# Kernel tuning notes

Measured on AMD Instinct MI355X. Metric: run time of the kernel, lower is better.

## Reference

```python
import jax, jax.numpy as jnp
import numpy as np

D_MODEL = 256
NUM_HEADS = 8
CURV = 1.0  # Poincare ball curvature c
EPS = 1e-5


def expmap0(v, c):
    # Exponential map at the origin of the Poincare ball.
    sqrt_c = jnp.sqrt(c)
    norm = jnp.sqrt(jnp.clip(jnp.sum(v * v, axis=-1, keepdims=True), 1e-12))
    return jnp.tanh(sqrt_c * norm) * v / (sqrt_c * norm)


def setup_inputs() -> dict:
    key = jax.random.key(0)
    ks = jax.random.split(key, 12)
    B, S, D = 2, 2048, D_MODEL
    s = 1.0 / np.sqrt(D)
    return {
        "x": jax.random.normal(ks[0], (B, S, D), dtype=jnp.float32),
        "Wq": jax.random.normal(ks[1], (D, D), dtype=jnp.float32) * s,
        "bq": jnp.zeros((D,), jnp.float32),
        "Wk": jax.random.normal(ks[2], (D, D), dtype=jnp.float32) * s,
        "bk": jnp.zeros((D,), jnp.float32),
        "Wv": jax.random.normal(ks[3], (D, D), dtype=jnp.float32) * s,
        "bv": jnp.zeros((D,), jnp.float32),
        "Wo": jax.random.normal(ks[4], (D, D), dtype=jnp.float32) * s,
        "bo": jnp.zeros((D,), jnp.float32),
        "Wfc": jax.random.normal(ks[5], (D, D), dtype=jnp.float32) * s,
        "bfc": jnp.zeros((D,), jnp.float32),
    }


def reference(x, Wq, bq, Wk, bk, Wv, bv, Wo, bo, Wfc, bfc):
    B, S, D = x.shape
    H, dh = NUM_HEADS, D // NUM_HEADS
    c = CURV

    def proj(W, b):
        return (x @ W.T + b).reshape(B, S, H, dh).transpose(0, 2, 1, 3)  # [B,H,S,dh]

    q = expmap0(proj(Wq, bq), c)
    k = expmap0(proj(Wk, bk), c)
    v = proj(Wv, bv)

    # Gram quantities; pairwise Poincare distance via closed-form Mobius-add norm.
    qq = jnp.sum(q * q, axis=-1)[..., :, None]          # [B,H,S,1]
    kk = jnp.sum(k * k, axis=-1)[..., None, :]          # [B,H,1,S]
    qk = jnp.einsum("bhsd,bhtd->bhst", q, k)            # [B,H,S,S]

    A = 1.0 - 2.0 * c * qk + c * kk
    Bc = 1.0 - c * qq
    den = 1.0 - 2.0 * c * qk + (c * c) * qq * kk
    num2 = A * A * qq + Bc * Bc * kk - 2.0 * A * Bc * qk  # ||(-q) mobius+ k||^2 * den^2
    n = jnp.sqrt(jnp.clip(num2, 0.0)) / jnp.clip(jnp.abs(den), 1e-12)
    sqrt_c = jnp.sqrt(c)
    dist = (2.0 / sqrt_c) * jnp.arctanh(jnp.clip(sqrt_c * n, 0.0, 1.0 - EPS))

    scores = -dist / np.sqrt(dh)
    attn = jax.nn.softmax(scores, axis=-1)
    out = jnp.einsum("bhst,bhtd->bhsd", attn, v)        # [B,H,S,dh]
    out = out.transpose(0, 2, 1, 3).reshape(B, S, D)
    out = out @ Wo.T + bo
    return out @ Wfc.T + bfc
```

## Files before the change

kernel.cpp:

```cpp
#include <hip/hip_runtime.h>
#include <cstdint>
#include <cstddef>


#define ALPHA 0.17677669529663687f
#define EMIN  -3.1129694f
#define CHI   1.95e-5f
#define NEG_INV_2CHI -25641.026f

typedef __bf16 bf16x8 __attribute__((ext_vector_type(8)));
typedef float  f32x4  __attribute__((ext_vector_type(4)));

__device__ __forceinline__ float fast_log2(float x) { return __builtin_amdgcn_logf(x); }
__device__ __forceinline__ float fast_exp2(float x) { return __builtin_amdgcn_exp2f(x); }

__global__ __launch_bounds__(256)
void k1_misc(const float* __restrict__ x,   const float* __restrict__ Wq,
             const float* __restrict__ Wk,  const float* __restrict__ Wv,
             const float* __restrict__ Wfc, const float* __restrict__ Wo,
             const float* __restrict__ bo,  const float* __restrict__ bfc,
             __bf16* __restrict__ xh, __bf16* __restrict__ xl,
             __bf16* __restrict__ Ws, __bf16* __restrict__ Wch,
             __bf16* __restrict__ Wcl, float* __restrict__ bcomb) {
  __shared__ float sh[2 * 32 * 68];
  const int bx = blockIdx.x, tid = threadIdx.x;
  if (bx < 16) {
    float (*AsT)[68] = (float(*)[68])sh;
    float (*Bs)[68]  = (float(*)[68])(sh + 32 * 68);
    const int ty = tid >> 4, tx = tid & 15;
    const int m0 = (bx >> 2) * 64, n0 = (bx & 3) * 64;
    float acc[4][4] = {};
    for (int k0 = 0; k0 < 256; k0 += 32) {
#pragma unroll
      for (int jj = 0; jj < 2; ++jj) {
        int j = tid * 2 + jj;
        {
          int r = j >> 3, c4 = (j & 7) << 2;
          float4 av = *(const float4*)&Wfc[(size_t)(m0 + r) * 256 + k0 + c4];
          AsT[c4 + 0][r] = av.x; AsT[c4 + 1][r] = av.y;
          AsT[c4 + 2][r] = av.z; AsT[c4 + 3][r] = av.w;
        }
        {
          int r = j >> 4, c4 = (j & 15) << 2;
          *(float4*)&Bs[r][c4] = *(const float4*)&Wo[(size_t)(k0 + r) * 256 + n0 + c4];
        }
      }
      __syncthreads();
#pragma unroll
      for (int kk = 0; kk < 32; ++kk) {
        float4 a = *(const float4*)&AsT[kk][ty * 4];
        float4 b = *(const float4*)&Bs[kk][tx * 4];
        float av[4] = {a.x, a.y, a.z, a.w};
        float bv[4] = {b.x, b.y, b.z, b.w};
#pragma unroll
        for (int i = 0; i < 4; ++i)
#pragma unroll
          for (int j2 = 0; j2 < 4; ++j2)
            acc[i][j2] = fmaf(av[i], bv[j2], acc[i][j2]);
      }
      __syncthreads();
    }
#pragma unroll
    for (int i = 0; i < 4; ++i) {
      union { __bf16 h[4]; uint2 u; } ph, pl;
#pragma unroll
      for (int j = 0; j < 4; ++j) {
        __bf16 hb = (__bf16)acc[i][j];
        ph.h[j] = hb;
        pl.h[j] = (__bf16)(acc[i][j] - (float)hb);
      }
      size_t off = (size_t)(m0 + ty * 4 + i) * 256 + n0 + tx * 4;
      *(uint2*)(Wch + off) = ph.u;
      *(uint2*)(Wcl + off) = pl.u;
    }
  } else if (bx < 32) {
    float* red = sh;
    int r = tid >> 4, c = tid & 15;
    int row = (bx - 16) * 16 + r;
    float s = 0.0f;
    for (int k = c; k < 256; k += 16) s = fmaf(Wfc[(size_t)row * 256 + k], bo[k], s);
    red[tid] = s;
    __syncthreads();
    if (c == 0) {
      float t = 0.0f;
#pragma unroll
      for (int i = 0; i < 16; ++i) t += red[r * 16 + i];
      bcomb[row] = t + bfc[row];
    }
  } else {
    int g = (bx - 32) * 256 + tid;
    const float* src;
    __bf16 *dh, *dl;
    if (g < 131072) {
      src = x + (size_t)g * 8; dh = xh + (size_t)g * 8; dl = xl + (size_t)g * 8;
    } else {
      int e = g - 131072;
      int wsel = e >> 13;
      int inner = (e & 8191) * 8;
      src = (wsel == 0 ? Wq : (wsel == 1 ? Wk : Wv)) + inner;
      dh = Ws + wsel * 131072 + inner;
      dl = Ws + wsel * 131072 + 65536 + inner;
    }
    union { __bf16 h[8]; uint4 u; } ph, pl;
#pragma unroll
    for (int i = 0; i < 2; ++i) {
      float4 v = *(const float4*)(src + i * 4);
      float vv[4] = {v.x, v.y, v.z, v.w};
#pragma unroll
      for (int j = 0; j < 4; ++j) {
        __bf16 hb = (__bf16)vv[j];
        ph.h[i * 4 + j] = hb;
        pl.h[i * 4 + j] = (__bf16)(vv[j] - (float)hb);
      }
    }
    *(uint4*)dh = ph.u;
    *(uint4*)dl = pl.u;
  }
}

__global__ __launch_bounds__(256)
void gemm_qkv_mfma(const __bf16* __restrict__ xh, const __bf16* __restrict__ xl,
                   const __bf16* __restrict__ Ws,
                   const float* __restrict__ bq, const float* __restrict__ bk,
                   const float* __restrict__ bv,
                   float* __restrict__ Qb, float* __restrict__ Kb,
                   float* __restrict__ Vb) {
  const int tid = threadIdx.x, w = tid >> 6, lane = tid & 63;
  const int l15 = lane & 15, lg = lane >> 4;
  const int m0 = blockIdx.x * 64, nb = blockIdx.y;
  const int wsel = nb >> 2;
  const int n256b = (nb & 3) * 64;
  const __bf16* Wh = Ws + wsel * 131072;
  const __bf16* Wl = Wh + 65536;
  const int arow = m0 + w * 16 + l15;
  const __bf16* axh = xh + (size_t)arow * 256 + lg * 8;
  const __bf16* axl = xl + (size_t)arow * 256 + lg * 8;
  f32x4 acc0 = {0,0,0,0}, acc1 = {0,0,0,0}, acc2 = {0,0,0,0}, acc3 = {0,0,0,0};
#pragma unroll
  for (int k0 = 0; k0 < 256; k0 += 32) {
    bf16x8 ah = *(const bf16x8*)(axh + k0);
    bf16x8 al = *(const bf16x8*)(axl + k0);
#pragma unroll
    for (int g = 0; g < 4; ++g) {
      const size_t br = (size_t)(n256b + g * 16 + l15) * 256 + lg * 8 + k0;
      bf16x8 bh = *(const bf16x8*)(Wh + br);
      bf16x8 bl = *(const bf16x8*)(Wl + br);
      f32x4& acc = g == 0 ? acc0 : (g == 1 ? acc1 : (g == 2 ? acc2 : acc3));
      acc = __builtin_amdgcn_mfma_f32_16x16x32_bf16(ah, bh, acc, 0, 0, 0);
      acc = __builtin_amdgcn_mfma_f32_16x16x32_bf16(al, bh, acc, 0, 0, 0);
      acc = __builtin_amdgcn_mfma_f32_16x16x32_bf16(ah, bl, acc, 0, 0, 0);
    }
  }
  const float* bias = wsel == 0 ? bq : (wsel == 1 ? bk : bv);
  float* C = wsel == 0 ? Qb : (wsel == 1 ? Kb : Vb);
#pragma unroll
  for (int g = 0; g < 4; ++g) {
    const f32x4& acc = g == 0 ? acc0 : (g == 1 ? acc1 : (g == 2 ? acc2 : acc3));
    int n256 = n256b + g * 16 + l15;
    float bval = bias[n256];
    int h = n256 >> 5, d = n256 & 31;
#pragma unroll
    for (int r = 0; r < 4; ++r) {
      int m = m0 + w * 16 + lg * 4 + r;
      int b = m >> 11, s = m & 2047;
      C[((size_t)((b << 3) + h) << 16) + (size_t)s * 32 + d] = acc[r] + bval;
    }
  }
}

__global__ __launch_bounds__(256)
void k3_prep(const float* __restrict__ Qf, const float* __restrict__ Kf,
             const float* __restrict__ Vf,
             __bf16* __restrict__ Qbf, __bf16* __restrict__ Kbf,
             __bf16* __restrict__ Vt,
             float4* __restrict__ qtab4, float4* __restrict__ ktab4,
             float* __restrict__ Vsum, float2* __restrict__ Kred) {
  __shared__ float2 red2[256];
  const int bx = blockIdx.x, tid = threadIdx.x;
  if (bx < 256) {
    int idx = bx * 256 + tid;
    const bool isQ = idx < 32768;
    const int i2 = isQ ? idx : idx - 32768;
    const float* src = (isQ ? Qf : Kf) + (size_t)i2 * 32;
    __bf16* dst = (isQ ? Qbf : Kbf) + (size_t)i2 * 32;
    float v[32];
    float ss = 0.0f;
#pragma unroll
    for (int i = 0; i < 8; ++i) {
      float4 v4 = *(const float4*)&src[i * 4];
      v[i*4+0] = v4.x; v[i*4+1] = v4.y; v[i*4+2] = v4.z; v[i*4+3] = v4.w;
      ss = fmaf(v4.x, v4.x, ss); ss = fmaf(v4.y, v4.y, ss);
      ss = fmaf(v4.z, v4.z, ss); ss = fmaf(v4.w, v4.w, ss);
    }
    ss = fmaxf(ss, 1e-12f);
    float x  = sqrtf(ss);
    float ex = fast_exp2(-2.8853900817779268f * x);
    float opex = 1.0f + ex;
    float th = (1.0f - ex) / opex;
    float sc = th / x;
    float qq = th * th;
    float Bv = 4.0f * ex / (opex * opex);
    float lgB = 2.0f - 2.8853900817779268f * x - 2.0f * fast_log2(opex);
    if (isQ) qtab4[i2] = float4{qq, ALPHA * lgB, Bv, 0.0f};
    else     ktab4[i2] = float4{qq, Bv, ALPHA * lgB, 0.0f};
    union { __bf16 h[8]; uint4 u; } pk;
#pragma unroll
    for (int blk = 0; blk < 4; ++blk) {
#pragma unroll
      for (int j = 0; j < 8; ++j) pk.h[j] = (__bf16)(v[blk * 8 + j] * sc);
      *(uint4*)(dst + blk * 8) = pk.u;
    }
    if (!isQ) {
      red2[tid] = float2{qq, Bv};
      __syncthreads();
      for (int s = 128; s > 0; s >>= 1) {
        if (tid < s) {
          red2[tid].x = fminf(red2[tid].x, red2[tid + s].x);
          red2[tid].y = fmaxf(red2[tid].y, red2[tid + s].y);
        }
        __syncthreads();
      }
      if (tid == 0) Kred[bx - 128] = red2[0];
    }
  } else if (bx < 768) {
    int g = (bx - 256) * 256 + tid;
    int bh = g >> 13, rem = g & 8191;
    int tb = rem >> 5, dh = rem & 31;
    const float* src = Vf + (((size_t)bh * 2048 + tb * 8) * 32) + dh;
    union { __bf16 h[8]; uint4 u; } pk;
#pragma unroll
    for (int e = 0; e < 8; ++e) pk.h[e] = (__bf16)src[e * 32];
    *(uint4*)(Vt + ((size_t)bh * 32 + dh) * 2048 + tb * 8) = pk.u;
  } else {
    int g = (bx - 768) * 256 + tid;
    int bh = g >> 11, rem = g & 2047;
    int t32 = rem >> 5, dh = rem & 31;
    const float* src = Vf + (((size_t)bh * 2048 + t32 * 32) * 32) + dh;
    float s = 0.0f;
#pragma unroll
    for (int j = 0; j < 32; ++j) s += src[j * 32];
    Vsum[((size_t)bh * 64 + t32) * 32 + dh] = s;
  }
}

__global__ __launch_bounds__(256)
void attn_mfma(const __bf16* __restrict__ Qbf, const __bf16* __restrict__ Kbf,
               const __bf16* __restrict__ Vt,  const float4* __restrict__ qtab4,
               const float4* __restrict__ ktab4, const float* __restrict__ Vsum,
               const float2* __restrict__ Kred,
               float* __restrict__ PN, float* __restrict__ PD) {
  __shared__ __bf16 Pt[4][16][72];
  const int tid = threadIdx.x;
  const int wid = tid >> 6, lane = tid & 63;
  const int l15 = lane & 15, lg = lane >> 4;
  const int tc = blockIdx.y, bh = blockIdx.z;
  const int sblk = blockIdx.x;
  const int s0 = sblk * 64 + wid * 16;

  bf16x8 qfrag = *(const bf16x8*)(Qbf + ((size_t)bh * 2048 + s0 + l15) * 32 + lg * 8);
  float4 qt = qtab4[bh * 2048 + s0 + l15];
  const float qq = qt.x, Bq = qt.z;
  const float eminRow = EMIN - qt.y;
  const float wclipf = (float)(__bf16)fast_exp2(eminRow);
  float wrow[4];
#pragma unroll
  for (int r = 0; r < 4; ++r)
    wrow[r] = (float)(__bf16)fast_exp2(EMIN - qtab4[bh * 2048 + s0 + lg * 4 + r].y);

  float kkmin = 1.0f, bkmax = 0.0f;
#pragma unroll
  for (int j = 0; j < 8; ++j) {
    float2 kr = Kred[bh * 8 + j];
    kkmin = fminf(kkmin, kr.x);
    bkmax = fmaxf(bkmax, kr.y);
  }
  const float thr_all = fmaf(0.5f * qq, kkmin,
                             fmaf(Bq * NEG_INV_2CHI, bkmax, 0.5f));

  const __bf16* Kbase = Kbf + ((size_t)bh << 16);
  const __bf16* Vbase = Vt + ((size_t)bh << 16);
  const float4* Tk = ktab4 + bh * 2048;
  const float*  VsBase = Vsum + (size_t)bh * 64 * 32;
  __bf16* Pw = &Pt[wid][0][0];

  f32x4 accO0 = {0.f, 0.f, 0.f, 0.f};
  f32x4 accO1 = {0.f, 0.f, 0.f, 0.f};
  float den = 0.0f;
  int nclip = 0;
  const f32x4 zero = {0.f, 0.f, 0.f, 0.f};
  const int tbeg = tc * 512;
  const int stag = sblk & 7;

  bf16x8 kfA0, kfA1, kfA2, kfA3, kfB0, kfB1, kfB2, kfB3;
  float vA0, vA1, vA2, vA3, vB0, vB1, vB2, vB3;

#define LOAD_SET(K0, K1, K2, K3, V0, V1, V2, V3, T0)                          \
  {                                                                           \
    const int _t = (T0);                                                      \
    K0 = *(const bf16x8*)(Kbase + (size_t)(_t + 0 * 16 + l15) * 32 + lg * 8); \
    K1 = *(const bf16x8*)(Kbase + (size_t)(_t + 1 * 16 + l15) * 32 + lg * 8); \
    K2 = *(const bf16x8*)(Kbase + (size_t)(_t + 2 * 16 + l15) * 32 + lg * 8); \
    K3 = *(const bf16x8*)(Kbase + (size_t)(_t + 3 * 16 + l15) * 32 + lg * 8); \
    const int _ti = _t >> 5;                                                  \
    V0 = VsBase[_ti * 32 + l15];                                              \
    V1 = VsBase[(_ti + 1) * 32 + l15];                                        \
    V2 = VsBase[_ti * 32 + 16 + l15];                                         \
    V3 = VsBase[(_ti + 1) * 32 + 16 + l15];                                   \
  }

#define COMPUTE_SET(K0, K1, K2, K3, V0, V1, V2, V3, T0)                       \
  {                                                                           \
    const int _t0 = (T0);                                                     \
    __builtin_amdgcn_s_setprio(1);                                            \
    _Pragma("unroll")                                                         \
    for (int h = 0; h < 2; ++h) {                                             \
      f32x4 S[2];                                                             \
      bool ok = true;                                                         \
      _Pragma("unroll")                                                       \
      for (int s2 = 0; s2 < 2; ++s2) {                                        \
        bf16x8 kf = (h == 0) ? (s2 == 0 ? K0 : K1) : (s2 == 0 ? K2 : K3);     \
        f32x4 Sv = __builtin_amdgcn_mfma_f32_16x16x32_bf16(kf, qfrag, zero,   \
                                                           0, 0, 0);          \
        S[s2] = Sv;                                                           \
        float m = fmaxf(fmaxf(Sv[0], Sv[1]), fmaxf(Sv[2], Sv[3]));            \
        ok &= (m <= thr_all);                                                 \
      }                                                                       \
      if (__all((int)ok)) {                                                   \
        ++nclip;                                                              \
        const float vsA = h ? V1 : V0;                                        \
        const float vsB = h ? V3 : V2;                                        \
        _Pragma("unroll")                                                     \
        for (int r = 0; r < 4; ++r) {                                         \
          accO0[r] = fmaf(wrow[r], vsA, accO0[r]);                            \
          accO1[r] = fmaf(wrow[r], vsB, accO1[r]);                            \
        }                                                                     \
      } else {                                                                \
        _Pragma("unroll")                                                     \
        for (int s2 = 0; s2 < 2; ++s2) {                                      \
          const int sub = h * 2 + s2;                                         \
          const int tk = _t0 + sub * 16 + lg * 4;                             \
          f32x4 Sv = S[s2];                                                   \
          float w[4];                                                         \
          _Pragma("unroll")                                                   \
          for (int r = 0; r < 4; ++r) {                                       \
            float4 T = Tk[tk + r];                                            \
            float qk2 = Sv[r] + Sv[r];                                        \
            float u = (qq + T.x) - qk2;                                       \
            float d = fmaf(qq, T.x, 1.0f) - qk2;                              \
            float p = fmaxf(u * d, 0.0f);                                     \
            float sq = sqrtf(p);                                              \
            float m2 = fmaf(2.0f, sq, u + d);                                 \
            float e = fmaf(-ALPHA, fast_log2(m2), T.z);                       \
            e = fmaxf(e, eminRow);                                            \
            w[r] = fast_exp2(e);                                              \
          }                                                                   \
          den += (w[0] + w[1]) + (w[2] + w[3]);                               \
          union { __bf16 hh[4]; uint2 u2; } pk;                               \
          pk.hh[0] = (__bf16)w[0]; pk.hh[1] = (__bf16)w[1];                   \
          pk.hh[2] = (__bf16)w[2]; pk.hh[3] = (__bf16)w[3];                   \
          *(uint2*)&Pw[l15 * 72 + sub * 16 + lg * 4] = pk.u2;                 \
        }                                                                     \
        bf16x8 pfrag = *(const bf16x8*)&Pw[l15 * 72 + h * 32 + lg * 8];       \
        bf16x8 v0 = *(const bf16x8*)(Vbase + (size_t)l15 * 2048 + _t0 +       \
                                     h * 32 + lg * 8);                        \
        bf16x8 v1 = *(const bf16x8*)(Vbase + (size_t)(16 + l15) * 2048 +      \
                                     _t0 + h * 32 + lg * 8);                  \
        accO0 = __builtin_amdgcn_mfma_f32_16x16x32_bf16(pfrag, v0, accO0,     \
                                                        0, 0, 0);             \
        accO1 = __builtin_amdgcn_mfma_f32_16x16x32_bf16(pfrag, v1, accO1,     \
                                                        0, 0, 0);             \
      }                                                                       \
    }                                                                         \
    __builtin_amdgcn_s_setprio(0);                                            \
  }

  LOAD_SET(kfA0, kfA1, kfA2, kfA3, vA0, vA1, vA2, vA3,
           tbeg + ((stag & 7) << 6));

#pragma unroll
  for (int i = 0; i < 8; ++i) {
    const int tcur = tbeg + (((i + stag) & 7) << 6);
    const int tnxt = tbeg + (((i + 1 + stag) & 7) << 6);
    if ((i & 1) == 0) {
      if (i < 7) LOAD_SET(kfB0, kfB1, kfB2, kfB3, vB0, vB1, vB2, vB3, tnxt);
      COMPUTE_SET(kfA0, kfA1, kfA2, kfA3, vA0, vA1, vA2, vA3, tcur);
    } else {
      if (i < 7) LOAD_SET(kfA0, kfA1, kfA2, kfA3, vA0, vA1, vA2, vA3, tnxt);
      COMPUTE_SET(kfB0, kfB1, kfB2, kfB3, vB0, vB1, vB2, vB3, tcur);
    }
  }
#undef LOAD_SET
#undef COMPUTE_SET

  den = fmaf(8.0f * wclipf, (float)nclip, den);
  den += __shfl_xor(den, 16);
  den += __shfl_xor(den, 32);
  size_t pbase = ((size_t)tc * 16 + bh) * 2048;
  if (lg == 0) PD[pbase + s0 + l15] = den;
#pragma unroll
  for (int r = 0; r < 4; ++r) {
    int sl = lg * 4 + r;
    size_t row = (pbase + s0 + sl) * 32;
    PN[row + l15]      = accO0[r];
    PN[row + 16 + l15] = accO1[r];
  }
}

__global__ __launch_bounds__(256)
void combine4(const float* __restrict__ PN, const float* __restrict__ PD,
              __bf16* __restrict__ AOh, __bf16* __restrict__ AOl) {
  int idx = blockIdx.x * 256 + threadIdx.x;
  int bh = idx >> 11, s = idx & 2047;
  int b = bh >> 3, h = bh & 7;
  float den = 0.0f;
#pragma unroll
  for (int c = 0; c < 4; ++c) den += PD[((size_t)c * 16 + bh) * 2048 + s];
  float r = 1.0f / den;
  size_t ob = ((size_t)b * 2048 + s) * 256 + h * 32;
#pragma unroll
  for (int i = 0; i < 8; ++i) {
    float4 sum = {0.0f, 0.0f, 0.0f, 0.0f};
#pragma unroll
    for (int c = 0; c < 4; ++c) {
      float4 v = *(const float4*)&PN[((((size_t)c * 16 + bh) * 2048 + s) * 32) + i * 4];
      sum.x += v.x; sum.y += v.y; sum.z += v.z; sum.w += v.w;
    }
    float vv[4] = {sum.x * r, sum.y * r, sum.z * r, sum.w * r};
    union { __bf16 h4[4]; uint2 u; } ph, pl;
#pragma unroll
    for (int j = 0; j < 4; ++j) {
      __bf16 hb = (__bf16)vv[j];
      ph.h4[j] = hb;
      pl.h4[j] = (__bf16)(vv[j] - (float)hb);
    }
    *(uint2*)(AOh + ob + i * 4) = ph.u;
    *(uint2*)(AOl + ob + i * 4) = pl.u;
  }
}

__global__ __launch_bounds__(256)
void gemm_out_mfma(const __bf16* __restrict__ aoh, const __bf16* __restrict__ aol,
                   const __bf16* __restrict__ Wch, const __bf16* __restrict__ Wcl,
                   const float* __restrict__ bcomb, float* __restrict__ out) {
  const int tid = threadIdx.x, w = tid >> 6, lane = tid & 63;
  const int l15 = lane & 15, lg = lane >> 4;
  const int m0 = blockIdx.x * 64, n0 = blockIdx.y * 64;
  const int arow = m0 + w * 16 + l15;
  const __bf16* axh = aoh + (size_t)arow * 256 + lg * 8;
  const __bf16* axl = aol + (size_t)arow * 256 + lg * 8;
  f32x4 acc0 = {0,0,0,0}, acc1 = {0,0,0,0}, acc2 = {0,0,0,0}, acc3 = {0,0,0,0};
#pragma unroll
  for (int k0 = 0; k0 < 256; k0 += 32) {
    bf16x8 ah = *(const bf16x8*)(axh + k0);
    bf16x8 al = *(const bf16x8*)(axl + k0);
#pragma unroll
    for (int g = 0; g < 4; ++g) {
      const size_t br = (size_t)(n0 + g * 16 + l15) * 256 + lg * 8 + k0;
      bf16x8 bh = *(const bf16x8*)(Wch + br);
      bf16x8 bl = *(const bf16x8*)(Wcl + br);
      f32x4& acc = g == 0 ? acc0 : (g == 1 ? acc1 : (g == 2 ? acc2 : acc3));
      acc = __builtin_amdgcn_mfma_f32_16x16x32_bf16(ah, bh, acc, 0, 0, 0);
      acc = __builtin_amdgcn_mfma_f32_16x16x32_bf16(al, bh, acc, 0, 0, 0);
      acc = __builtin_amdgcn_mfma_f32_16x16x32_bf16(ah, bl, acc, 0, 0, 0);
    }
  }
#pragma unroll
  for (int g = 0; g < 4; ++g) {
    const f32x4& acc = g == 0 ? acc0 : (g == 1 ? acc1 : (g == 2 ? acc2 : acc3));
    int n = n0 + g * 16 + l15;
    float bval = bcomb[n];
#pragma unroll
    for (int r = 0; r < 4; ++r) {
      int m = m0 + w * 16 + lg * 4 + r;
      out[(size_t)m * 256 + n] = acc[r] + bval;
    }
  }
}

extern "C" void kernel_launch(void* const* d_in, const int* in_sizes, int n_in,
                              void* d_out, int out_size, void* d_ws, size_t ws_size,
                              hipStream_t stream) {
  const float* x   = (const float*)d_in[0];
  const float* Wq  = (const float*)d_in[1];
  const float* bq  = (const float*)d_in[2];
  const float* Wk  = (const float*)d_in[3];
  const float* bk  = (const float*)d_in[4];
  const float* Wv  = (const float*)d_in[5];
  const float* bv  = (const float*)d_in[6];
  const float* Wo  = (const float*)d_in[7];
  const float* bo  = (const float*)d_in[8];
  const float* Wfc = (const float*)d_in[9];
  const float* bfc = (const float*)d_in[10];

  float* ws = (float*)d_ws;
  float* Qb  = ws;
  float* Kb  = ws + (1 << 20);
  float* Vb  = ws + (2 << 20);
  __bf16* Qbf = (__bf16*)(ws + (3 << 20));
  __bf16* Kbf = (__bf16*)(ws + (3 << 20) + (1 << 19));
  __bf16* Vtb = (__bf16*)(ws + (4 << 20));
  float4* qtab4 = (float4*)(ws + (4 << 20) + (1 << 19));
  float4* ktab4 = (float4*)(ws + (4 << 20) + (1 << 19) + (1 << 17));
  float*  Vsum  = ws + (4 << 20) + (1 << 19) + (2 << 17);
  __bf16* Wch   = (__bf16*)(Vsum + (1 << 15));
  __bf16* Wcl   = Wch + 65536;
  float*  bcomb = Vsum + (1 << 15) + (1 << 16);
  float2* Kred  = (float2*)(bcomb + 256);
  __bf16* xh = (__bf16*)(ws + (5 << 20));
  __bf16* xl = (__bf16*)(ws + (5 << 20) + (1 << 19));
  __bf16* Wsplit = (__bf16*)(ws + (6 << 20));
  float* PN = ws + (6 << 20) + (1 << 18);
  float* PD = PN + (4 << 20);
  __bf16* AOh = (__bf16*)ws;
  __bf16* AOl = (__bf16*)(ws + (1 << 19));

  dim3 blk(256);
  k1_misc<<<dim3(640), blk, 0, stream>>>(x, Wq, Wk, Wv, Wfc, Wo, bo, bfc,
                                         xh, xl, Wsplit, Wch, Wcl, bcomb);
  gemm_qkv_mfma<<<dim3(64, 12), blk, 0, stream>>>(xh, xl, Wsplit, bq, bk, bv,
                                                  Qb, Kb, Vb);
  k3_prep<<<dim3(896), blk, 0, stream>>>(Qb, Kb, Vb, Qbf, Kbf, Vtb,
                                         qtab4, ktab4, Vsum, Kred);
  attn_mfma<<<dim3(32, 4, 16), blk, 0, stream>>>(Qbf, Kbf, Vtb, qtab4, ktab4,
                                                 Vsum, Kred, PN, PD);
  combine4<<<dim3(128), blk, 0, stream>>>(PN, PD, AOh, AOl);
  gemm_out_mfma<<<dim3(64, 4), blk, 0, stream>>>(AOh, AOl, Wch, Wcl, bcomb,
                                                 (float*)d_out);
}
```

Baseline: 110.1 us.

## Fuse expmap0 Q/K prep into QKV GEMM epilogue and store partials in bf16

The QKV GEMM epilogue now applies the bias and computes per-head norms with cross-lane shuffles. It then applies the expmap0 scaling and writes bf16 Q/K, the q/k tables and the K min/max reduction directly, so fp32 Q/K no longer round-trip through global memory. The V transpose and sum move to a smaller dedicated kernel. Attention partial numerators are stored as bf16 instead of fp32, halving combine traffic but adding rounding error in the partial sums.

Result: faster. 105.8 us (-3.9%).

```diff
diff --git a/kernel.cpp b/kernel.cpp
--- a/kernel.cpp
+++ b/kernel.cpp
@@ -7,6 +7,7 @@
 #define EMIN  -3.1129694f
 #define CHI   1.95e-5f
 #define NEG_INV_2CHI -25641.026f
+#define TWOLOG2E 2.8853900817779268f
 
 typedef __bf16 bf16x8 __attribute__((ext_vector_type(8)));
 typedef float  f32x4  __attribute__((ext_vector_type(4)));
@@ -123,8 +124,11 @@
                    const __bf16* __restrict__ Ws,
                    const float* __restrict__ bq, const float* __restrict__ bk,
                    const float* __restrict__ bv,
-                   float* __restrict__ Qb, float* __restrict__ Kb,
-                   float* __restrict__ Vb) {
+                   __bf16* __restrict__ Qbf, __bf16* __restrict__ Kbf,
+                   float* __restrict__ Vb,
+                   float4* __restrict__ qtab4, float4* __restrict__ ktab4,
+                   float2* __restrict__ Kred) {
+  __shared__ float4 kredsh[4];
   const int tid = threadIdx.x, w = tid >> 6, lane = tid & 63;
   const int l15 = lane & 15, lg = lane >> 4;
   const int m0 = blockIdx.x * 64, nb = blockIdx.y;
@@ -152,78 +156,125 @@
     }
   }
   const float* bias = wsel == 0 ? bq : (wsel == 1 ? bk : bv);
-  float* C = wsel == 0 ? Qb : (wsel == 1 ? Kb : Vb);
-#pragma unroll
-  for (int g = 0; g < 4; ++g) {
-    const f32x4& acc = g == 0 ? acc0 : (g == 1 ? acc1 : (g == 2 ? acc2 : acc3));
-    int n256 = n256b + g * 16 + l15;
-    float bval = bias[n256];
-    int h = n256 >> 5, d = n256 & 31;
+
+  if (wsel == 2) {
+#pragma unroll
+    for (int g = 0; g < 4; ++g) {
+      const f32x4& acc = g == 0 ? acc0 : (g == 1 ? acc1 : (g == 2 ? acc2 : acc3));
+      int n256 = n256b + g * 16 + l15;
+      float bval = bias[n256];
+      int h = n256 >> 5, d = n256 & 31;
+#pragma unroll
+      for (int r = 0; r < 4; ++r) {
+        int m = m0 + w * 16 + lg * 4 + r;
+        int b = m >> 11, s = m & 2047;
+        Vb[((size_t)((b << 3) + h) << 16) + (size_t)s * 32 + d] = acc[r] + bval;
+      }
+    }
+    return;
+  }
+
+  const float bv0 = bias[n256b + 0 * 16 + l15];
+  const float bv1 = bias[n256b + 1 * 16 + l15];
+  const float bv2 = bias[n256b + 2 * 16 + l15];
+  const float bv3 = bias[n256b + 3 * 16 + l15];
+  float ssA[4], ssB[4];
+#pragma unroll
+  for (int r = 0; r < 4; ++r) {
+    acc0[r] += bv0; acc1[r] += bv1; acc2[r] += bv2; acc3[r] += bv3;
+    ssA[r] = acc0[r] * acc0[r] + acc1[r] * acc1[r];
+    ssB[r] = acc2[r] * acc2[r] + acc3[r] * acc3[r];
+  }
+#pragma unroll
+  for (int mk = 1; mk < 16; mk <<= 1) {
 #pragma unroll
     for (int r = 0; r < 4; ++r) {
-      int m = m0 + w * 16 + lg * 4 + r;
-      int b = m >> 11, s = m & 2047;
-      C[((size_t)((b << 3) + h) << 16) + (size_t)s * 32 + d] = acc[r] + bval;
+      ssA[r] += __shfl_xor(ssA[r], mk);
+      ssB[r] += __shfl_xor(ssB[r], mk);
+    }
+  }
+  float scA[4], qqA[4], BvA[4], lgA[4];
+  float scB[4], qqB[4], BvB[4], lgB_[4];
+#pragma unroll
+  for (int r = 0; r < 4; ++r) {
+    {
+      float ss = fmaxf(ssA[r], 1e-12f);
+      float xv = sqrtf(ss);
+      float ex = fast_exp2(-TWOLOG2E * xv);
+      float opex = 1.0f + ex;
+      float th = (1.0f - ex) / opex;
+      scA[r] = th / xv;
+      qqA[r] = th * th;
+      BvA[r] = 4.0f * ex / (opex * opex);
+      lgA[r] = 2.0f - TWOLOG2E * xv - 2.0f * fast_log2(opex);
+    }
+    {
+      float ss = fmaxf(ssB[r], 1e-12f);
+      float xv = sqrtf(ss);
+      float ex = fast_exp2(-TWOLOG2E * xv);
+      float opex = 1.0f + ex;
+      float th = (1.0f - ex) / opex;
+      scB[r] = th / xv;
+      qqB[r] = th * th;
+      BvB[r] = 4.0f * ex / (opex * opex);
+      lgB_[r] = 2.0f - TWOLOG2E * xv - 2.0f * fast_log2(opex);
+    }
+  }
+  __bf16* dst = wsel == 0 ? Qbf : Kbf;
+  float4* tab = wsel == 0 ? qtab4 : ktab4;
+  const int b = m0 >> 11;
+  const int headA = n256b >> 5, headB = headA + 1;
+  const int bhA = (b << 3) + headA, bhB = (b << 3) + headB;
+  const int sbase = (m0 & 2047) + w * 16 + lg * 4;
+#pragma unroll
+  for (int r = 0; r < 4; ++r) {
+    int s = sbase + r;
+    size_t baseA = ((size_t)bhA * 2048 + s) * 32;
+    size_t baseB = ((size_t)bhB * 2048 + s) * 32;
+    dst[baseA + l15]      = (__bf16)(acc0[r] * scA[r]);
+    dst[baseA + 16 + l15] = (__bf16)(acc1[r] * scA[r]);
+    dst[baseB + l15]      = (__bf16)(acc2[r] * scB[r]);
+    dst[baseB + 16 + l15] = (__bf16)(acc3[r] * scB[r]);
+    if (l15 == 0) {
+      if (wsel == 0) {
+        tab[(size_t)bhA * 2048 + s] = float4{qqA[r], ALPHA * lgA[r], BvA[r], 0.0f};
+        tab[(size_t)bhB * 2048 + s] = float4{qqB[r], ALPHA * lgB_[r], BvB[r], 0.0f};
+      } else {
+        tab[(size_t)bhA * 2048 + s] = float4{qqA[r], BvA[r], ALPHA * lgA[r], 0.0f};
+        tab[(size_t)bhB * 2048 + s] = float4{qqB[r], BvB[r], ALPHA * lgB_[r], 0.0f};
+      }
+    }
+  }
+  if (wsel == 1) {
+    float mnA = fminf(fminf(qqA[0], qqA[1]), fminf(qqA[2], qqA[3]));
+    float mxA = fmaxf(fmaxf(BvA[0], BvA[1]), fmaxf(BvA[2], BvA[3]));
+    float mnB = fminf(fminf(qqB[0], qqB[1]), fminf(qqB[2], qqB[3]));
+    float mxB = fmaxf(fmaxf(BvB[0], BvB[1]), fmaxf(BvB[2], BvB[3]));
+    mnA = fminf(mnA, __shfl_xor(mnA, 16)); mnA = fminf(mnA, __shfl_xor(mnA, 32));
+    mxA = fmaxf(mxA, __shfl_xor(mxA, 16)); mxA = fmaxf(mxA, __shfl_xor(mxA, 32));
+    mnB = fminf(mnB, __shfl_xor(mnB, 16)); mnB = fminf(mnB, __shfl_xor(mnB, 32));
+    mxB = fmaxf(mxB, __shfl_xor(mxB, 16)); mxB = fmaxf(mxB, __shfl_xor(mxB, 32));
+    if (lane == 0) kredsh[w] = float4{mnA, mxA, mnB, mxB};
+    __syncthreads();
+    if (tid == 0) {
+      float4 a = kredsh[0], b4 = kredsh[1], c4 = kredsh[2], d4 = kredsh[3];
+      float MnA = fminf(fminf(a.x, b4.x), fminf(c4.x, d4.x));
+      float MxA = fmaxf(fmaxf(a.y, b4.y), fmaxf(c4.y, d4.y));
+      float MnB = fminf(fminf(a.z, b4.z), fminf(c4.z, d4.z));
+      float MxB = fmaxf(fmaxf(a.w, b4.w), fmaxf(c4.w, d4.w));
+      int bx31 = blockIdx.x & 31;
+      Kred[bhA * 32 + bx31] = float2{MnA, MxA};
+      Kred[bhB * 32 + bx31] = float2{MnB, MxB};
     }
   }
 }
 
 __global__ __launch_bounds__(256)
-void k3_prep(const float* __restrict__ Qf, const float* __restrict__ Kf,
-             const float* __restrict__ Vf,
-             __bf16* __restrict__ Qbf, __bf16* __restrict__ Kbf,
-             __bf16* __restrict__ Vt,
-             float4* __restrict__ qtab4, float4* __restrict__ ktab4,
-             float* __restrict__ Vsum, float2* __restrict__ Kred) {
-  __shared__ float2 red2[256];
+void k3v(const float* __restrict__ Vf, __bf16* __restrict__ Vt,
+         float* __restrict__ Vsum) {
   const int bx = blockIdx.x, tid = threadIdx.x;
-  if (bx < 256) {
-    int idx = bx * 256 + tid;
-    const bool isQ = idx < 32768;
-    const int i2 = isQ ? idx : idx - 32768;
-    const float* src = (isQ ? Qf : Kf) + (size_t)i2 * 32;
-    __bf16* dst = (isQ ? Qbf : Kbf) + (size_t)i2 * 32;
-    float v[32];
-    float ss = 0.0f;
-#pragma unroll
-    for (int i = 0; i < 8; ++i) {
-      float4 v4 = *(const float4*)&src[i * 4];
-      v[i*4+0] = v4.x; v[i*4+1] = v4.y; v[i*4+2] = v4.z; v[i*4+3] = v4.w;
-      ss = fmaf(v4.x, v4.x, ss); ss = fmaf(v4.y, v4.y, ss);
-      ss = fmaf(v4.z, v4.z, ss); ss = fmaf(v4.w, v4.w, ss);
-    }
-    ss = fmaxf(ss, 1e-12f);
-    float x  = sqrtf(ss);
-    float ex = fast_exp2(-2.8853900817779268f * x);
-    float opex = 1.0f + ex;
-    float th = (1.0f - ex) / opex;
-    float sc = th / x;
-    float qq = th * th;
-    float Bv = 4.0f * ex / (opex * opex);
-    float lgB = 2.0f - 2.8853900817779268f * x - 2.0f * fast_log2(opex);
-    if (isQ) qtab4[i2] = float4{qq, ALPHA * lgB, Bv, 0.0f};
-    else     ktab4[i2] = float4{qq, Bv, ALPHA * lgB, 0.0f};
-    union { __bf16 h[8]; uint4 u; } pk;
-#pragma unroll
-    for (int blk = 0; blk < 4; ++blk) {
-#pragma unroll
-      for (int j = 0; j < 8; ++j) pk.h[j] = (__bf16)(v[blk * 8 + j] * sc);
-      *(uint4*)(dst + blk * 8) = pk.u;
-    }
-    if (!isQ) {
-      red2[tid] = float2{qq, Bv};
-      __syncthreads();
-      for (int s = 128; s > 0; s >>= 1) {
-        if (tid < s) {
-          red2[tid].x = fminf(red2[tid].x, red2[tid + s].x);
-          red2[tid].y = fmaxf(red2[tid].y, red2[tid + s].y);
-        }
-        __syncthreads();
-      }
-      if (tid == 0) Kred[bx - 128] = red2[0];
-    }
-  } else if (bx < 768) {
-    int g = (bx - 256) * 256 + tid;
+  if (bx < 512) {
+    int g = bx * 256 + tid;
     int bh = g >> 13, rem = g & 8191;
     int tb = rem >> 5, dh = rem & 31;
     const float* src = Vf + (((size_t)bh * 2048 + tb * 8) * 32) + dh;
@@ -232,7 +283,7 @@
     for (int e = 0; e < 8; ++e) pk.h[e] = (__bf16)src[e * 32];
     *(uint4*)(Vt + ((size_t)bh * 32 + dh) * 2048 + tb * 8) = pk.u;
   } else {
-    int g = (bx - 768) * 256 + tid;
+    int g = (bx - 512) * 256 + tid;
     int bh = g >> 11, rem = g & 2047;
     int t32 = rem >> 5, dh = rem & 31;
     const float* src = Vf + (((size_t)bh * 2048 + t32 * 32) * 32) + dh;
@@ -248,7 +299,7 @@
                const __bf16* __restrict__ Vt,  const float4* __restrict__ qtab4,
                const float4* __restrict__ ktab4, const float* __restrict__ Vsum,
                const float2* __restrict__ Kred,
-               float* __restrict__ PN, float* __restrict__ PD) {
+               __bf16* __restrict__ PNb, float* __restrict__ PD) {
   __shared__ __bf16 Pt[4][16][72];
   const int tid = threadIdx.x;
   const int wid = tid >> 6, lane = tid & 63;
@@ -269,8 +320,8 @@
 
   float kkmin = 1.0f, bkmax = 0.0f;
 #pragma unroll
-  for (int j = 0; j < 8; ++j) {
-    float2 kr = Kred[bh * 8 + j];
+  for (int j = 0; j < 32; ++j) {
+    float2 kr = Kred[bh * 32 + j];
     kkmin = fminf(kkmin, kr.x);
     bkmax = fmaxf(bkmax, kr.y);
   }
@@ -401,13 +452,13 @@
   for (int r = 0; r < 4; ++r) {
     int sl = lg * 4 + r;
     size_t row = (pbase + s0 + sl) * 32;
-    PN[row + l15]      = accO0[r];
-    PN[row + 16 + l15] = accO1[r];
+    PNb[row + l15]      = (__bf16)accO0[r];
+    PNb[row + 16 + l15] = (__bf16)accO1[r];
   }
 }
 
 __global__ __launch_bounds__(256)
-void combine4(const float* __restrict__ PN, const float* __restrict__ PD,
+void combine4(const __bf16* __restrict__ PNb, const float* __restrict__ PD,
               __bf16* __restrict__ AOh, __bf16* __restrict__ AOl) {
   int idx = blockIdx.x * 256 + threadIdx.x;
   int bh = idx >> 11, s = idx & 2047;
@@ -418,23 +469,24 @@
   float r = 1.0f / den;
   size_t ob = ((size_t)b * 2048 + s) * 256 + h * 32;
 #pragma unroll
-  for (int i = 0; i < 8; ++i) {
-    float4 sum = {0.0f, 0.0f, 0.0f, 0.0f};
+  for (int i = 0; i < 4; ++i) {
+    float acc8[8] = {};
 #pragma unroll
     for (int c = 0; c < 4; ++c) {
-      float4 v = *(const float4*)&PN[((((size_t)c * 16 + bh) * 2048 + s) * 32) + i * 4];
-      sum.x += v.x; sum.y += v.y; sum.z += v.z; sum.w += v.w;
-    }
-    float vv[4] = {sum.x * r, sum.y * r, sum.z * r, sum.w * r};
-    union { __bf16 h4[4]; uint2 u; } ph, pl;
-#pragma unroll
-    for (int j = 0; j < 4; ++j) {
-      __bf16 hb = (__bf16)vv[j];
-      ph.h4[j] = hb;
-      pl.h4[j] = (__bf16)(vv[j] - (float)hb);
-    }
-    *(uint2*)(AOh + ob + i * 4) = ph.u;
-    *(uint2*)(AOl + ob + i * 4) = pl.u;
+      bf16x8 v = *(const bf16x8*)&PNb[((((size_t)c * 16 + bh) * 2048 + s) * 32) + i * 8];
+#pragma unroll
+      for (int j = 0; j < 8; ++j) acc8[j] += (float)v[j];
+    }
+    union { __bf16 h8[8]; uint4 u; } ph, pl;
+#pragma unroll
+    for (int j = 0; j < 8; ++j) {
+      float val = acc8[j] * r;
+      __bf16 hb = (__bf16)val;
+      ph.h8[j] = hb;
+      pl.h8[j] = (__bf16)(val - (float)hb);
+    }
+    *(uint4*)(AOh + ob + i * 8) = ph.u;
+    *(uint4*)(AOl + ob + i * 8) = pl.u;
   }
 }
 
@@ -493,8 +545,6 @@
   const float* bfc = (const float*)d_in[10];
 
   float* ws = (float*)d_ws;
-  float* Qb  = ws;
-  float* Kb  = ws + (1 << 20);
   float* Vb  = ws + (2 << 20);
   __bf16* Qbf = (__bf16*)(ws + (3 << 20));
   __bf16* Kbf = (__bf16*)(ws + (3 << 20) + (1 << 19));
@@ -509,8 +559,8 @@
   __bf16* xh = (__bf16*)(ws + (5 << 20));
   __bf16* xl = (__bf16*)(ws + (5 << 20) + (1 << 19));
   __bf16* Wsplit = (__bf16*)(ws + (6 << 20));
-  float* PN = ws + (6 << 20) + (1 << 18);
-  float* PD = PN + (4 << 20);
+  __bf16* PNb = (__bf16*)(ws + (6 << 20) + (1 << 18));
+  float* PD = ws + (6 << 20) + (1 << 18) + (2 << 20);
   __bf16* AOh = (__bf16*)ws;
   __bf16* AOl = (__bf16*)(ws + (1 << 19));
 
@@ -518,12 +568,12 @@
   k1_misc<<<dim3(640), blk, 0, stream>>>(x, Wq, Wk, Wv, Wfc, Wo, bo, bfc,
                                          xh, xl, Wsplit, Wch, Wcl, bcomb);
   gemm_qkv_mfma<<<dim3(64, 12), blk, 0, stream>>>(xh, xl, Wsplit, bq, bk, bv,
-                                                  Qb, Kb, Vb);
-  k3_prep<<<dim3(896), blk, 0, stream>>>(Qb, Kb, Vb, Qbf, Kbf, Vtb,
-                                         qtab4, ktab4, Vsum, Kred);
+                                                  Qbf, Kbf, Vb, qtab4, ktab4,
+                                                  Kred);
+  k3v<<<dim3(640), blk, 0, stream>>>(Vb, Vtb, Vsum);
   attn_mfma<<<dim3(32, 4, 16), blk, 0, stream>>>(Qbf, Kbf, Vtb, qtab4, ktab4,
-                                                 Vsum, Kred, PN, PD);
-  combine4<<<dim3(128), blk, 0, stream>>>(PN, PD, AOh, AOl);
+                                                 Vsum, Kred, PNb, PD);
+  combine4<<<dim3(128), blk, 0, stream>>>(PNb, PD, AOh, AOl);
   gemm_out_mfma<<<dim3(64, 4), blk, 0, stream>>>(AOh, AOl, Wch, Wcl, bcomb,
                                                  (float*)d_out);
 }
```
